# Kernel tuning notes

Measured on AMD Instinct MI355X. Metric: run time of the kernel, lower is better.

Reference implementation:

```python
import jax, jax.numpy as jnp
import numpy as np

N = 100000   # nodes
E = 800000   # edges
IN, H, OUT = 128, 128, 100  # in_channels, hidden_channels, out_channels


def _layernorm(x, g, b, eps=1e-5):
    m = jnp.mean(x, axis=-1, keepdims=True)
    v = jnp.var(x, axis=-1, keepdims=True)
    return (x - m) * jax.lax.rsqrt(v + eps) * g + b


def _sage_mean(x, src, dst, wl, bl, wr, n):
    # PyG SAGEConv(aggr='mean'): lin_l(mean_j x_j) + lin_r(x)
    s = jax.ops.segment_sum(x[src], dst, num_segments=n)               # [n, d]
    cnt = jax.ops.segment_sum(jnp.ones_like(dst, jnp.float32), dst, num_segments=n)
    aggr = s / jnp.maximum(cnt, 1.0)[:, None]
    return aggr @ wl + bl + x @ wr


def _sage_max(x, src, dst, wl, bl, wr, n):
    # PyG SAGEConv(aggr='max'): lin_l(max_j x_j) + lin_r(x); empty segments -> 0
    m = jax.ops.segment_max(x[src], dst, num_segments=n)               # [n, d]
    m = jnp.where(jnp.isfinite(m), m, 0.0)
    return m @ wl + bl + x @ wr


def setup_inputs() -> dict:
    key = jax.random.key(0)
    ks = jax.random.split(key, 16)

    def w(k, shape):
        fan_in = shape[0]
        return jax.random.normal(k, shape, jnp.float32) * (1.0 / np.sqrt(fan_in))

    inp = {
        'x': jax.random.normal(ks[0], (N, IN), jnp.float32),
        'src': jax.random.randint(ks[1], (E,), 0, N, jnp.int32),
        'dst': jax.random.randint(ks[2], (E,), 0, N, jnp.int32),
        's1_wl': w(ks[3], (IN, H)), 's1_bl': jnp.zeros((H,), jnp.float32), 's1_wr': w(ks[4], (IN, H)),
        'ln1_g': jnp.ones((H,), jnp.float32), 'ln1_b': jnp.zeros((H,), jnp.float32),
        's2_wl': w(ks[5], (H, 2 * H)), 's2_bl': jnp.zeros((2 * H,), jnp.float32), 's2_wr': w(ks[6], (H, 2 * H)),
        'ln2_g': jnp.ones((2 * H,), jnp.float32), 'ln2_b': jnp.zeros((2 * H,), jnp.float32),
        's3_wl': w(ks[7], (2 * H, H)), 's3_bl': jnp.zeros((H,), jnp.float32), 's3_wr': w(ks[8], (2 * H, H)),
        'ln3_g': jnp.ones((H,), jnp.float32), 'ln3_b': jnp.zeros((H,), jnp.float32),
        'l1_w': w(ks[9], (H, H // 2)), 'l1_b': jnp.zeros((H // 2,), jnp.float32),
        'ln4_g': jnp.ones((H // 2,), jnp.float32), 'ln4_b': jnp.zeros((H // 2,), jnp.float32),
        'lo_w': w(ks[10], (H // 2, OUT)), 'lo_b': jnp.zeros((OUT,), jnp.float32),
    }
    return inp


def reference(x, src, dst,
              s1_wl, s1_bl, s1_wr, ln1_g, ln1_b,
              s2_wl, s2_bl, s2_wr, ln2_g, ln2_b,
              s3_wl, s3_bl, s3_wr, ln3_g, ln3_b,
              l1_w, l1_b, ln4_g, ln4_b, lo_w, lo_b):
    n = x.shape[0]
    h = _sage_mean(x, src, dst, s1_wl, s1_bl, s1_wr, n)
    h = jax.nn.relu(_layernorm(h, ln1_g, ln1_b))          # dropout disabled (eval)
    h = _sage_max(h, src, dst, s2_wl, s2_bl, s2_wr, n)
    h = jax.nn.relu(_layernorm(h, ln2_g, ln2_b))
    h = _sage_mean(h, src, dst, s3_wl, s3_bl, s3_wr, n)
    h = jax.nn.relu(_layernorm(h, ln3_g, ln3_b))
    h = h @ l1_w + l1_b
    h = jax.nn.relu(_layernorm(h, ln4_g, ln4_b))
    return h @ lo_w + lo_b                                 # [N, OUT]
```

## Files before the change

kernel.cpp:

```cpp
#include <hip/hip_runtime.h>
#include <stdint.h>

#define DEV __device__ __forceinline__

typedef __attribute__((ext_vector_type(8))) short bf16x8;
typedef __attribute__((ext_vector_type(4))) float f32x4;

DEV float bf2f(uint16_t u) { return __uint_as_float(((uint32_t)u) << 16); }
DEV uint16_t f2bfbits(float f) {
    uint32_t x = __float_as_uint(f);
    uint32_t r = x + 0x7fffu + ((x >> 16) & 1u);
    return (uint16_t)(r >> 16);
}
DEV void stv(uint16_t* p, float v) { *p = f2bfbits(v); }
DEV void stv(float* p, float v) { *p = v; }

template<int C> DEV void ldbf(const uint16_t* p, float* f);
template<> DEV void ldbf<2>(const uint16_t* p, float* f) {
    uint32_t v = *reinterpret_cast<const uint32_t*>(p);
    f[0] = __uint_as_float(v << 16); f[1] = __uint_as_float(v & 0xffff0000u);
}
template<> DEV void ldbf<4>(const uint16_t* p, float* f) {
    uint2 v = *reinterpret_cast<const uint2*>(p);
    f[0] = __uint_as_float(v.x << 16); f[1] = __uint_as_float(v.x & 0xffff0000u);
    f[2] = __uint_as_float(v.y << 16); f[3] = __uint_as_float(v.y & 0xffff0000u);
}
template<> DEV void ldbf<8>(const uint16_t* p, float* f) {
    uint4 v = *reinterpret_cast<const uint4*>(p);
    f[0] = __uint_as_float(v.x << 16); f[1] = __uint_as_float(v.x & 0xffff0000u);
    f[2] = __uint_as_float(v.y << 16); f[3] = __uint_as_float(v.y & 0xffff0000u);
    f[4] = __uint_as_float(v.z << 16); f[5] = __uint_as_float(v.z & 0xffff0000u);
    f[6] = __uint_as_float(v.w << 16); f[7] = __uint_as_float(v.w & 0xffff0000u);
}

DEV void gl16(const uint16_t* g, uint8_t* l) {
    __builtin_amdgcn_global_load_lds(
        (const __attribute__((address_space(1))) uint32_t*)g,
        (__attribute__((address_space(3))) uint32_t*)l, 16, 0, 0);
}

template<int N> DEV void vwait() {
    if constexpr (N == 0)      asm volatile("s_waitcnt vmcnt(0)" ::: "memory");
    else if constexpr (N == 3) asm volatile("s_waitcnt vmcnt(3)" ::: "memory");
    else if constexpr (N == 4) asm volatile("s_waitcnt vmcnt(4)" ::: "memory");
    else if constexpr (N == 6) asm volatile("s_waitcnt vmcnt(6)" ::: "memory");
    else                       asm volatile("s_waitcnt vmcnt(0)" ::: "memory");
}

__global__ void k_count(const int* __restrict__ dst, int e, int* __restrict__ deg) {
    int i = blockIdx.x * 256 + threadIdx.x;
    if (i < e) atomicAdd(&deg[dst[i]], 1);
}

__global__ void k_block_sums(const int* __restrict__ deg, int n, int* __restrict__ bsum) {
    __shared__ int sm[256];
    int base = blockIdx.x * 1024;
    int s = 0;
    for (int i = threadIdx.x; i < 1024; i += 256) {
        int g = base + i;
        if (g < n) s += deg[g];
    }
    sm[threadIdx.x] = s; __syncthreads();
    for (int o = 128; o > 0; o >>= 1) {
        if (threadIdx.x < o) sm[threadIdx.x] += sm[threadIdx.x + o];
        __syncthreads();
    }
    if (threadIdx.x == 0) bsum[blockIdx.x] = sm[0];
}

__global__ void k_scan_bsums(int* bsum, int nb) {
    __shared__ int sm[256];
    int t = threadIdx.x;
    int v = (t < nb) ? bsum[t] : 0;
    sm[t] = v; __syncthreads();
    for (int o = 1; o < 256; o <<= 1) {
        int add = (t >= o) ? sm[t - o] : 0;
        __syncthreads();
        sm[t] += add;
        __syncthreads();
    }
    if (t < nb) bsum[t] = (t == 0) ? 0 : sm[t - 1];
}

__global__ void k_scan_final(const int* __restrict__ deg, int n,
                             const int* __restrict__ bsum, int* __restrict__ offs,
                             int* __restrict__ cursor) {
    __shared__ int sm[256];
    int t = threadIdx.x;
    int i0 = blockIdx.x * 1024 + t * 4;
    int d0 = (i0     < n) ? deg[i0]     : 0;
    int d1 = (i0 + 1 < n) ? deg[i0 + 1] : 0;
    int d2 = (i0 + 2 < n) ? deg[i0 + 2] : 0;
    int d3 = (i0 + 3 < n) ? deg[i0 + 3] : 0;
    int ts = d0 + d1 + d2 + d3;
    sm[t] = ts; __syncthreads();
    for (int o = 1; o < 256; o <<= 1) {
        int add = (t >= o) ? sm[t - o] : 0;
        __syncthreads();
        sm[t] += add;
        __syncthreads();
    }
    int e0 = bsum[blockIdx.x] + ((t == 0) ? 0 : sm[t - 1]);
    int e1 = e0 + d0, e2 = e1 + d1, e3 = e2 + d2, e4 = e3 + d3;
    if (i0     < n) { offs[i0]     = e0; cursor[i0]     = e0; }
    if (i0 + 1 < n) { offs[i0 + 1] = e1; cursor[i0 + 1] = e1; }
    if (i0 + 2 < n) { offs[i0 + 2] = e2; cursor[i0 + 2] = e2; }
    if (i0 + 3 < n) { offs[i0 + 3] = e3; cursor[i0 + 3] = e3; }
    if (i0 <= n - 1 && n - 1 < i0 + 4) offs[n] = e4;
}

__global__ void k_scatter(const int* __restrict__ src, const int* __restrict__ dst, int e,
                          int* __restrict__ cursor, int* __restrict__ csr) {
    int i = blockIdx.x * 256 + threadIdx.x;
    if (i < e) {
        int p = atomicAdd(&cursor[dst[i]], 1);
        csr[p] = src[i];
    }
}

__global__ void k_f2b(const float* __restrict__ in, uint16_t* __restrict__ o, int n4) {
    int i = blockIdx.x * 256 + threadIdx.x;
    if (i < n4) {
        float4 v = reinterpret_cast<const float4*>(in)[i];
        uint2 w;
        w.x = f2bfbits(v.x) | ((uint32_t)f2bfbits(v.y) << 16);
        w.y = f2bfbits(v.z) | ((uint32_t)f2bfbits(v.w) << 16);
        reinterpret_cast<uint2*>(o)[i] = w;
    }
}

struct PrepSeg { const float* W; uint16_t* wt; int K, Dreal, ncols, koff, noff, Dtot, start, end; };
struct PrepAll { PrepSeg s[8]; };

__global__ void k_prep_all(PrepAll P, int total) {
    int idx = blockIdx.x * 256 + threadIdx.x;
    if (idx >= total) return;
#pragma unroll
    for (int i = 0; i < 8; ++i) {
        if (idx >= P.s[i].start && idx < P.s[i].end) {
            int loc = idx - P.s[i].start;
            int K = P.s[i].K;
            int nn = loc / K, k = loc - nn * K;
            float v = (nn < P.s[i].Dreal) ? P.s[i].W[(size_t)k * P.s[i].Dreal + nn] : 0.f;
            int c = P.s[i].noff + nn;
            int kk = P.s[i].koff + k;
            P.s[i].wt[((size_t)(kk >> 3) * P.s[i].Dtot + c) * 8 + (kk & 7)] = f2bfbits(v);
        }
    }
}

__global__ __launch_bounds__(256) void k_aggr_max(const uint16_t* __restrict__ X,
                                                  const int* __restrict__ offs,
                                                  const int* __restrict__ csr,
                                                  int n, uint16_t* __restrict__ out) {
    int sl = threadIdx.x & 15;
    int node = blockIdx.x * 16 + (threadIdx.x >> 4);
    if (node >= n) return;
    int beg = offs[node], end = offs[node + 1];
    float acc[8] = {};
    const size_t loff = (size_t)sl * 8;
    int i = beg;
    for (; i + 3 < end; i += 4) {
        int s0 = csr[i], s1 = csr[i + 1], s2 = csr[i + 2], s3 = csr[i + 3];
        float f0[8], f1[8], f2[8], f3[8];
        ldbf<8>(X + (size_t)s0 * 128 + loff, f0);
        ldbf<8>(X + (size_t)s1 * 128 + loff, f1);
        ldbf<8>(X + (size_t)s2 * 128 + loff, f2);
        ldbf<8>(X + (size_t)s3 * 128 + loff, f3);
#pragma unroll
        for (int c = 0; c < 8; c++)
            acc[c] = fmaxf(acc[c], fmaxf(fmaxf(f0[c], f1[c]), fmaxf(f2[c], f3[c])));
    }
    for (; i < end; ++i) {
        int s = csr[i];
        float f[8];
        ldbf<8>(X + (size_t)s * 128 + loff, f);
#pragma unroll
        for (int c = 0; c < 8; c++) acc[c] = fmaxf(acc[c], f[c]);
    }
    uint4 v;
    v.x = f2bfbits(acc[0]) | ((uint32_t)f2bfbits(acc[1]) << 16);
    v.y = f2bfbits(acc[2]) | ((uint32_t)f2bfbits(acc[3]) << 16);
    v.z = f2bfbits(acc[4]) | ((uint32_t)f2bfbits(acc[5]) << 16);
    v.w = f2bfbits(acc[6]) | ((uint32_t)f2bfbits(acc[7]) << 16);
    *reinterpret_cast<uint4*>(out + (size_t)node * 128 + loff) = v;
}

__global__ __launch_bounds__(256) void k_aggr_ln(const uint16_t* __restrict__ YZ,
                                                 const int* __restrict__ offs,
                                                 const int* __restrict__ csr,
                                                 const float* __restrict__ g,
                                                 const float* __restrict__ b,
                                                 int n, uint16_t* __restrict__ out) {
    int sl = threadIdx.x & 15;
    int node = blockIdx.x * 16 + (threadIdx.x >> 4);
    if (node >= n) return;
    int beg = offs[node], end = offs[node + 1];
    float a[8] = {};
    const size_t loff = (size_t)sl * 8;
    int i = beg;
    for (; i + 3 < end; i += 4) {
        int s0 = csr[i], s1 = csr[i + 1], s2 = csr[i + 2], s3 = csr[i + 3];
        float f0[8], f1[8], f2[8], f3[8];
        ldbf<8>(YZ + (size_t)s0 * 256 + loff, f0);
        ldbf<8>(YZ + (size_t)s1 * 256 + loff, f1);
        ldbf<8>(YZ + (size_t)s2 * 256 + loff, f2);
        ldbf<8>(YZ + (size_t)s3 * 256 + loff, f3);
#pragma unroll
        for (int c = 0; c < 8; c++) a[c] += (f0[c] + f1[c]) + (f2[c] + f3[c]);
    }
    for (; i < end; ++i) {
        int s = csr[i];
        float f[8];
        ldbf<8>(YZ + (size_t)s * 256 + loff, f);
#pragma unroll
        for (int c = 0; c < 8; c++) a[c] += f[c];
    }
    int d = end - beg; if (d < 1) d = 1;
    float scale = 1.f / (float)d;
    float z[8];
    ldbf<8>(YZ + (size_t)node * 256 + 128 + loff, z);
    float v[8];
#pragma unroll
    for (int c = 0; c < 8; c++) v[c] = a[c] * scale + z[c];
    float s = 0.f, s2 = 0.f;
#pragma unroll
    for (int c = 0; c < 8; c++) { s += v[c]; s2 += v[c] * v[c]; }
#pragma unroll
    for (int o = 1; o < 16; o <<= 1) { s += __shfl_xor(s, o); s2 += __shfl_xor(s2, o); }
    float mean = s * (1.f / 128.f);
    float var = s2 * (1.f / 128.f) - mean * mean;
    float inv = rsqrtf(var + 1e-5f);
    float y[8];
#pragma unroll
    for (int c = 0; c < 8; c++)
        y[c] = fmaxf((v[c] - mean) * inv * g[loff + c] + b[loff + c], 0.f);
    uint4 w;
    w.x = f2bfbits(y[0]) | ((uint32_t)f2bfbits(y[1]) << 16);
    w.y = f2bfbits(y[2]) | ((uint32_t)f2bfbits(y[3]) << 16);
    w.z = f2bfbits(y[4]) | ((uint32_t)f2bfbits(y[5]) << 16);
    w.w = f2bfbits(y[6]) | ((uint32_t)f2bfbits(y[7]) << 16);
    *reinterpret_cast<uint4*>(out + (size_t)node * 128 + loff) = w;
}

template<int KPER, int DOUT, int DB, bool DUAL, bool LN, bool ZBIAS, typename TO>
__global__ __launch_bounds__(256) void k_mf(const uint16_t* __restrict__ A0,
                                            const uint16_t* __restrict__ A1,
                                            const uint16_t* __restrict__ WT,
                                            const float* __restrict__ bias,
                                            const float* __restrict__ g,
                                            const float* __restrict__ bvec,
                                            int n, TO* __restrict__ out) {
    constexpr int KEFF = KPER * (DUAL ? 2 : 1);
    constexpr int NST = KEFF / 32;
    constexpr int NF = DB / 16;
    constexpr int WPL = DB * 16;
    constexpr int AB = 8192;
    constexpr int WB = DB * 64;
    constexpr int HB = DB / 64;
    constexpr int L  = 2 + HB;
    __shared__ __align__(16) uint8_t lds[3][AB + WB];

    int tid = threadIdx.x;
    int lane = tid & 63, wid = tid >> 6;
    int lr = lane & 15, kb = lane >> 4;
    int row0 = blockIdx.x * 128;
    int wrow = wid * 32;

    auto stage = [&](int kt, uint8_t* buf) {
        const uint16_t* Asel = A0; int kk = kt;
        if (DUAL && kt >= KPER) { Asel = A1; kk = kt - KPER; }
        uint8_t* aB = buf;
        uint8_t* wB = buf + AB;
#pragma unroll
        for (int j = 0; j < 2; ++j) {
            int p = wid * 2 + j, cb = p >> 1, h = p & 1;
            int grow = row0 + h * 64 + lane; if (grow >= n) grow = n - 1;
            gl16(Asel + (size_t)grow * KPER + kk + cb * 8, aB + cb * 2048 + h * 1024);
        }
#pragma unroll
        for (int j = 0; j < HB; ++j) {
            int p = wid * HB + j, cb = p / HB, h = p % HB;
            int plane = (kt >> 3) + cb;
            gl16(WT + ((size_t)plane * DB + h * 64 + lane) * 8, wB + cb * WPL + h * 1024);
        }
    };

    f32x4 acc[2][NF] = {};
    stage(0, lds[0]);
    if constexpr (NST > 1) stage(32, lds[1]);

#pragma unroll
    for (int s = 0; s < NST; ++s) {
        if (s < NST - 1) vwait<L>(); else vwait<0>();
        __builtin_amdgcn_s_barrier();
        __builtin_amdgcn_sched_barrier(0);
        if (s + 2 < NST) stage((s + 2) * 32, lds[(s + 2) % 3]);
        const uint8_t* aB = lds[s % 3];
        const uint8_t* wB = lds[s % 3] + AB;
        bf16x8 af0 = *reinterpret_cast<const bf16x8*>(aB + kb * 2048 + (wrow + lr) * 16);
        bf16x8 af1 = *reinterpret_cast<const bf16x8*>(aB + kb * 2048 + (wrow + 16 + lr) * 16);
#pragma unroll
        for (int nf = 0; nf < NF; ++nf) {
            bf16x8 wf = *reinterpret_cast<const bf16x8*>(wB + kb * WPL + (nf * 16 + lr) * 16);
            acc[0][nf] = __builtin_amdgcn_mfma_f32_16x16x32_bf16(af0, wf, acc[0][nf], 0, 0, 0);
            acc[1][nf] = __builtin_amdgcn_mfma_f32_16x16x32_bf16(af1, wf, acc[1][nf], 0, 0, 0);
        }
    }

#pragma unroll
    for (int nf = 0; nf < NF; ++nf) {
        int col = nf * 16 + lr;
        float bsv;
        if constexpr (ZBIAS) {
            bsv = (col >= DOUT / 2) ? bias[col - DOUT / 2] : 0.f;
        } else {
            bsv = (DB == DOUT || col < DOUT) ? bias[col] : 0.f;
        }
#pragma unroll
        for (int r = 0; r < 4; ++r) { acc[0][nf][r] += bsv; acc[1][nf][r] += bsv; }
    }
    if constexpr (LN) {
        float gv[NF], bv2[NF];
#pragma unroll
        for (int nf = 0; nf < NF; ++nf) {
            int col = nf * 16 + lr;
            gv[nf] = g[col]; bv2[nf] = bvec[col];
        }
#pragma unroll
        for (int m = 0; m < 2; ++m) {
            float s[4], s2[4];
#pragma unroll
            for (int r = 0; r < 4; ++r) { s[r] = 0.f; s2[r] = 0.f; }
#pragma unroll
            for (int nf = 0; nf < NF; ++nf)
#pragma unroll
                for (int r = 0; r < 4; ++r) { float v = acc[m][nf][r]; s[r] += v; s2[r] += v * v; }
#pragma unroll
            for (int r = 0; r < 4; ++r) {
#pragma unroll
                for (int o = 1; o < 16; o <<= 1) {
                    s[r] += __shfl_xor(s[r], o);
                    s2[r] += __shfl_xor(s2[r], o);
                }
                float mean = s[r] / DOUT;
                float var = s2[r] / DOUT - mean * mean;
                float inv = rsqrtf(var + 1e-5f);
#pragma unroll
                for (int nf = 0; nf < NF; ++nf) {
                    float y = (acc[m][nf][r] - mean) * inv * gv[nf] + bv2[nf];
                    acc[m][nf][r] = fmaxf(y, 0.f);
                }
            }
        }
    }
#pragma unroll
    for (int m = 0; m < 2; ++m)
#pragma unroll
        for (int r = 0; r < 4; ++r) {
            int row = row0 + wrow + m * 16 + kb * 4 + r;
            if (row < n) {
#pragma unroll
                for (int nf = 0; nf < NF; ++nf) {
                    int col = nf * 16 + lr;
                    if (DB == DOUT || col < DOUT)
                        stv(out + (size_t)row * DOUT + col, acc[m][nf][r]);
                }
            }
        }
}

__global__ __launch_bounds__(256) void k_tail(const uint16_t* __restrict__ A,
                                              const uint16_t* __restrict__ WT4,
                                              const float* __restrict__ b4,
                                              const float* __restrict__ g4,
                                              const float* __restrict__ bv4,
                                              const uint16_t* __restrict__ WT5,
                                              const float* __restrict__ b5,
                                              int n, float* __restrict__ out) {
    __shared__ __align__(16) uint8_t lds[3][8192 + 4096];
    __shared__ __align__(16) uint8_t w5L[16384];
    __shared__ __align__(16) uint8_t h4L[16384];

    int tid = threadIdx.x;
    int lane = tid & 63, wid = tid >> 6;
    int lr = lane & 15, kb = lane >> 4;
    int row0 = blockIdx.x * 128;
    int wrow = wid * 32;

    auto stage = [&](int kt, uint8_t* buf) {
        uint8_t* aB = buf;
        uint8_t* wB = buf + 8192;
#pragma unroll
        for (int j = 0; j < 2; ++j) {
            int p = wid * 2 + j, cb = p >> 1, h = p & 1;
            int grow = row0 + h * 64 + lane; if (grow >= n) grow = n - 1;
            gl16(A + (size_t)grow * 128 + kt + cb * 8, aB + cb * 2048 + h * 1024);
        }
        gl16(WT4 + ((size_t)((kt >> 3) + wid) * 64 + lane) * 8, wB + wid * 1024);
    };

#pragma unroll
    for (int j = 0; j < 4; ++j) {
        int p = wid * 4 + j, cb = p >> 1, h = p & 1;
        gl16(WT5 + ((size_t)cb * 128 + h * 64 + lane) * 8, w5L + cb * 2048 + h * 1024);
    }

    f32x4 acc1[2][4] = {};
    stage(0, lds[0]);
    stage(32, lds[1]);

#pragma unroll
    for (int s = 0; s < 4; ++s) {
        if (s < 3) vwait<3>(); else vwait<0>();
        __builtin_amdgcn_s_barrier();
        __builtin_amdgcn_sched_barrier(0);
        if (s + 2 < 4) stage((s + 2) * 32, lds[(s + 2) % 3]);
        const uint8_t* aB = lds[s % 3];
        const uint8_t* wB = lds[s % 3] + 8192;
        bf16x8 af0 = *reinterpret_cast<const bf16x8*>(aB + kb * 2048 + (wrow + lr) * 16);
        bf16x8 af1 = *reinterpret_cast<const bf16x8*>(aB + kb * 2048 + (wrow + 16 + lr) * 16);
#pragma unroll
        for (int nf = 0; nf < 4; ++nf) {
            bf16x8 wf = *reinterpret_cast<const bf16x8*>(wB + kb * 1024 + (nf * 16 + lr) * 16);
            acc1[0][nf] = __builtin_amdgcn_mfma_f32_16x16x32_bf16(af0, wf, acc1[0][nf], 0, 0, 0);
            acc1[1][nf] = __builtin_amdgcn_mfma_f32_16x16x32_bf16(af1, wf, acc1[1][nf], 0, 0, 0);
        }
    }

#pragma unroll
    for (int nf = 0; nf < 4; ++nf) {
        float bsv = b4[nf * 16 + lr];
#pragma unroll
        for (int r = 0; r < 4; ++r) { acc1[0][nf][r] += bsv; acc1[1][nf][r] += bsv; }
    }
    {
        float gv[4], bv2[4];
#pragma unroll
        for (int nf = 0; nf < 4; ++nf) { gv[nf] = g4[nf * 16 + lr]; bv2[nf] = bv4[nf * 16 + lr]; }
#pragma unroll
        for (int m = 0; m < 2; ++m) {
            float s[4] = {}, s2[4] = {};
#pragma unroll
            for (int nf = 0; nf < 4; ++nf)
#pragma unroll
                for (int r = 0; r < 4; ++r) { float v = acc1[m][nf][r]; s[r] += v; s2[r] += v * v; }
#pragma unroll
            for (int r = 0; r < 4; ++r) {
#pragma unroll
                for (int o = 1; o < 16; o <<= 1) { s[r] += __shfl_xor(s[r], o); s2[r] += __shfl_xor(s2[r], o); }
                float mean = s[r] * (1.f / 64.f);
                float var = s2[r] * (1.f / 64.f) - mean * mean;
                float inv = rsqrtf(var + 1e-5f);
#pragma unroll
                for (int nf = 0; nf < 4; ++nf)
                    acc1[m][nf][r] = fmaxf((acc1[m][nf][r] - mean) * inv * gv[nf] + bv2[nf], 0.f);
            }
        }
    }

#pragma unroll
    for (int m = 0; m < 2; ++m)
#pragma unroll
        for (int r = 0; r < 4; ++r) {
            int row = wrow + m * 16 + kb * 4 + r;
#pragma unroll
            for (int nf = 0; nf < 4; ++nf) {
                int col = nf * 16 + lr;
                *reinterpret_cast<uint16_t*>(h4L + ((col >> 3) * 2048 + row * 16 + (col & 7) * 2)) =
                    f2bfbits(acc1[m][nf][r]);
            }
        }
    __syncthreads();

    f32x4 acc2[2][8] = {};
#pragma unroll
    for (int s = 0; s < 2; ++s) {
        bf16x8 af0 = *reinterpret_cast<const bf16x8*>(h4L + (s * 4 + kb) * 2048 + (wrow + lr) * 16);
        bf16x8 af1 = *reinterpret_cast<const bf16x8*>(h4L + (s * 4 + kb) * 2048 + (wrow + 16 + lr) * 16);
#pragma unroll
        for (int nf = 0; nf < 8; ++nf) {
            bf16x8 wf = *reinterpret_cast<const bf16x8*>(w5L + (s * 4 + kb) * 2048 + (nf * 16 + lr) * 16);
            acc2[0][nf] = __builtin_amdgcn_mfma_f32_16x16x32_bf16(af0, wf, acc2[0][nf], 0, 0, 0);
            acc2[1][nf] = __builtin_amdgcn_mfma_f32_16x16x32_bf16(af1, wf, acc2[1][nf], 0, 0, 0);
        }
    }
#pragma unroll
    for (int m = 0; m < 2; ++m)
#pragma unroll
        for (int r = 0; r < 4; ++r) {
            int row = row0 + wrow + m * 16 + kb * 4 + r;
            if (row < n) {
#pragma unroll
                for (int nf = 0; nf < 8; ++nf) {
                    int col = nf * 16 + lr;
                    if (col < 100)
                        out[(size_t)row * 100 + col] = acc2[m][nf][r] + b5[col];
                }
            }
        }
}

extern "C" void kernel_launch(void* const* d_in, const int* in_sizes, int n_in,
                              void* d_out, int out_size, void* d_ws, size_t ws_size,
                              hipStream_t stream) {
    const float* x     = (const float*)d_in[0];
    const int*   src   = (const int*)d_in[1];
    const int*   dst   = (const int*)d_in[2];
    const float* s1_wl = (const float*)d_in[3];
    const float* s1_bl = (const float*)d_in[4];
    const float* s1_wr = (const float*)d_in[5];
    const float* ln1_g = (const float*)d_in[6];
    const float* ln1_b = (const float*)d_in[7];
    const float* s2_wl = (const float*)d_in[8];
    const float* s2_bl = (const float*)d_in[9];
    const float* s2_wr = (const float*)d_in[10];
    const float* ln2_g = (const float*)d_in[11];
    const float* ln2_b = (const float*)d_in[12];
    const float* s3_wl = (const float*)d_in[13];
    const float* s3_bl = (const float*)d_in[14];
    const float* s3_wr = (const float*)d_in[15];
    const float* ln3_g = (const float*)d_in[16];
    const float* ln3_b = (const float*)d_in[17];
    const float* l1_w  = (const float*)d_in[18];
    const float* l1_b  = (const float*)d_in[19];
    const float* ln4_g = (const float*)d_in[20];
    const float* ln4_b = (const float*)d_in[21];
    const float* lo_w  = (const float*)d_in[22];
    const float* lo_b  = (const float*)d_in[23];
    float* out = (float*)d_out;

    const int N = in_sizes[0] / 128;
    const int E = in_sizes[1];
    (void)n_in; (void)out_size; (void)ws_size;

    char* w = (char*)d_ws;
    size_t off = 0;
    auto alloc = [&](size_t bytes) -> void* {
        void* p = w + off;
        off = (off + bytes + 255) & ~(size_t)255;
        return p;
    };
    int* deg    = (int*)alloc((size_t)N * 4);
    int* offs   = (int*)alloc((size_t)(N + 1) * 4);
    int* cursor = (int*)alloc((size_t)N * 4);
    int* bsum   = (int*)alloc(1024 * 4);
    int* csr    = (int*)alloc((size_t)E * 4);
    uint16_t* wt1 = (uint16_t*)alloc(256 * 128 * 2);
    uint16_t* wt2 = (uint16_t*)alloc(256 * 256 * 2);
    uint16_t* wt3 = (uint16_t*)alloc(256 * 256 * 2);
    uint16_t* wt4 = (uint16_t*)alloc(64 * 128 * 2);
    uint16_t* wt5 = (uint16_t*)alloc(128 * 64 * 2);
    uint16_t* xb    = (uint16_t*)alloc((size_t)N * 128 * 2);
    uint16_t* YZ    = (uint16_t*)alloc((size_t)N * 256 * 2);
    uint16_t* h1    = (uint16_t*)alloc((size_t)N * 128 * 2);
    uint16_t* aggrB = (uint16_t*)alloc((size_t)N * 128 * 2);
    uint16_t* h2    = (uint16_t*)alloc((size_t)N * 256 * 2);
    uint16_t* h3    = (uint16_t*)alloc((size_t)N * 128 * 2);

    int gE = (E + 255) / 256;
    int nb = (N + 1023) / 1024;
    int gN16 = (N + 15) / 16;
    int g128 = (N + 127) / 128;

    hipMemsetAsync(deg, 0, (size_t)N * 4, stream);
    k_count<<<gE, 256, 0, stream>>>(dst, E, deg);
    k_block_sums<<<nb, 256, 0, stream>>>(deg, N, bsum);
    k_scan_bsums<<<1, 256, 0, stream>>>(bsum, nb);
    k_scan_final<<<nb, 256, 0, stream>>>(deg, N, bsum, offs, cursor);
    k_scatter<<<gE, 256, 0, stream>>>(src, dst, E, cursor, csr);

    PrepAll P;
    int cum = 0;
    auto seg = [&](int i, const float* W, uint16_t* wt, int K, int Dreal, int ncols,
                   int koff, int noff, int Dtot) {
        P.s[i] = {W, wt, K, Dreal, ncols, koff, noff, Dtot, cum, cum + ncols * K};
        cum += ncols * K;
    };
    seg(0, s1_wl, wt1, 128, 128, 128, 0,   0,   256);
    seg(1, s1_wr, wt1, 128, 128, 128, 0,   128, 256);
    seg(2, s2_wl, wt2, 128, 256, 256, 0,   0,   256);
    seg(3, s2_wr, wt2, 128, 256, 256, 128, 0,   256);
    seg(4, s3_wl, wt3, 256, 128, 128, 0,   0,   256);
    seg(5, s3_wr, wt3, 256, 128, 128, 0,   128, 256);
    seg(6, l1_w,  wt4, 128, 64,  64,  0,   0,   64);
    seg(7, lo_w,  wt5, 64,  100, 128, 0,   0,   128);
    k_prep_all<<<(cum + 255) / 256, 256, 0, stream>>>(P, cum);

    k_f2b<<<(N * 128 / 4 + 255) / 256, 256, 0, stream>>>(x, xb, N * 128 / 4);

    k_mf<128, 256, 256, false, false, true, uint16_t><<<g128, 256, 0, stream>>>(
        xb, nullptr, wt1, s1_bl, nullptr, nullptr, N, YZ);
    k_aggr_ln<<<gN16, 256, 0, stream>>>(YZ, offs, csr, ln1_g, ln1_b, N, h1);

    k_aggr_max<<<gN16, 256, 0, stream>>>(h1, offs, csr, N, aggrB);
    k_mf<128, 256, 256, true, true, false, uint16_t><<<g128, 256, 0, stream>>>(
        aggrB, h1, wt2, s2_bl, ln2_g, ln2_b, N, h2);

    k_mf<256, 256, 256, false, false, true, uint16_t><<<g128, 256, 0, stream>>>(
        h2, nullptr, wt3, s3_bl, nullptr, nullptr, N, YZ);
    k_aggr_ln<<<gN16, 256, 0, stream>>>(YZ, offs, csr, ln3_g, ln3_b, N, h3);

    k_tail<<<g128, 256, 0, stream>>>(h3, wt4, l1_b, ln4_g, ln4_b, wt5, lo_b, N, out);
}
```

Measured before the change: 347.3 us.

## Preload whole swizzled A row panel into LDS and halve GEMM block rows

```diff
diff --git a/kernel.cpp b/kernel.cpp
--- a/kernel.cpp
+++ b/kernel.cpp
@@ -16,15 +16,6 @@
 DEV void stv(float* p, float v) { *p = v; }
 
 template<int C> DEV void ldbf(const uint16_t* p, float* f);
-template<> DEV void ldbf<2>(const uint16_t* p, float* f) {
-    uint32_t v = *reinterpret_cast<const uint32_t*>(p);
-    f[0] = __uint_as_float(v << 16); f[1] = __uint_as_float(v & 0xffff0000u);
-}
-template<> DEV void ldbf<4>(const uint16_t* p, float* f) {
-    uint2 v = *reinterpret_cast<const uint2*>(p);
-    f[0] = __uint_as_float(v.x << 16); f[1] = __uint_as_float(v.x & 0xffff0000u);
-    f[2] = __uint_as_float(v.y << 16); f[3] = __uint_as_float(v.y & 0xffff0000u);
-}
 template<> DEV void ldbf<8>(const uint16_t* p, float* f) {
     uint4 v = *reinterpret_cast<const uint4*>(p);
     f[0] = __uint_as_float(v.x << 16); f[1] = __uint_as_float(v.x & 0xffff0000u);
@@ -243,7 +234,7 @@
     *reinterpret_cast<uint4*>(out + (size_t)node * 128 + loff) = w;
 }
 
-template<int KPER, int DOUT, int DB, bool DUAL, bool LN, bool ZBIAS, typename TO>
+template<int KPER, int DOUT, bool DUAL, bool LN, bool ZBIAS, typename TO>
 __global__ __launch_bounds__(256) void k_mf(const uint16_t* __restrict__ A0,
                                             const uint16_t* __restrict__ A1,
                                             const uint16_t* __restrict__ WT,
@@ -251,60 +242,71 @@
                                             const float* __restrict__ g,
                                             const float* __restrict__ bvec,
                                             int n, TO* __restrict__ out) {
+    constexpr int DB = 256;
     constexpr int KEFF = KPER * (DUAL ? 2 : 1);
     constexpr int NST = KEFF / 32;
     constexpr int NF = DB / 16;
     constexpr int WPL = DB * 16;
-    constexpr int AB = 8192;
     constexpr int WB = DB * 64;
     constexpr int HB = DB / 64;
-    constexpr int L  = 2 + HB;
-    __shared__ __align__(16) uint8_t lds[3][AB + WB];
+    constexpr int RB = KPER * 2;
+    constexpr int PAN = 64 * RB;
+    constexpr int PCH = PAN / 1024;
+    constexpr int NPAN = DUAL ? 2 : 1;
+    __shared__ __align__(16) uint8_t aP[NPAN * PAN];
+    __shared__ __align__(16) uint8_t wL[3][WB];
 
     int tid = threadIdx.x;
     int lane = tid & 63, wid = tid >> 6;
     int lr = lane & 15, kb = lane >> 4;
-    int row0 = blockIdx.x * 128;
-    int wrow = wid * 32;
-
-    auto stage = [&](int kt, uint8_t* buf) {
-        const uint16_t* Asel = A0; int kk = kt;
-        if (DUAL && kt >= KPER) { Asel = A1; kk = kt - KPER; }
-        uint8_t* aB = buf;
-        uint8_t* wB = buf + AB;
-#pragma unroll
-        for (int j = 0; j < 2; ++j) {
-            int p = wid * 2 + j, cb = p >> 1, h = p & 1;
-            int grow = row0 + h * 64 + lane; if (grow >= n) grow = n - 1;
-            gl16(Asel + (size_t)grow * KPER + kk + cb * 8, aB + cb * 2048 + h * 1024);
-        }
+    int row0 = blockIdx.x * 64;
+
+    for (int c = wid; c < NPAN * PCH; c += 4) {
+        int pan = c / PCH, cc = c % PCH;
+        const uint16_t* Asrc = (DUAL && pan) ? A1 : A0;
+        int rloc, colb;
+        if constexpr (RB == 256) { rloc = cc * 4 + (lane >> 4); colb = (lane & 15) * 16; }
+        else                     { rloc = cc * 2 + (lane >> 5); colb = (lane & 31) * 16; }
+        int grow = row0 + rloc; if (grow >= n) grow = n - 1;
+        gl16((const uint16_t*)((const uint8_t*)Asrc + (size_t)grow * RB + (colb ^ ((rloc & 7) << 4))),
+             aP + (size_t)c * 1024);
+    }
+
+    auto stageW = [&](int kt, uint8_t* buf) {
 #pragma unroll
         for (int j = 0; j < HB; ++j) {
             int p = wid * HB + j, cb = p / HB, h = p % HB;
             int plane = (kt >> 3) + cb;
-            gl16(WT + ((size_t)plane * DB + h * 64 + lane) * 8, wB + cb * WPL + h * 1024);
+            gl16(WT + ((size_t)plane * DB + h * 64 + lane) * 8, buf + cb * WPL + h * 1024);
         }
     };
 
-    f32x4 acc[2][NF] = {};
-    stage(0, lds[0]);
-    if constexpr (NST > 1) stage(32, lds[1]);
-
+    stageW(0, wL[0]);
+    if constexpr (NST > 1) stageW(32, wL[1]);
+    vwait<0>();
+    __builtin_amdgcn_s_barrier();
+    __builtin_amdgcn_sched_barrier(0);
+
+    f32x4 acc[NF] = {};
 #pragma unroll
     for (int s = 0; s < NST; ++s) {
-        if (s < NST - 1) vwait<L>(); else vwait<0>();
-        __builtin_amdgcn_s_barrier();
-        __builtin_amdgcn_sched_barrier(0);
-        if (s + 2 < NST) stage((s + 2) * 32, lds[(s + 2) % 3]);
-        const uint8_t* aB = lds[s % 3];
-        const uint8_t* wB = lds[s % 3] + AB;
-        bf16x8 af0 = *reinterpret_cast<const bf16x8*>(aB + kb * 2048 + (wrow + lr) * 16);
-        bf16x8 af1 = *reinterpret_cast<const bf16x8*>(aB + kb * 2048 + (wrow + 16 + lr) * 16);
+        if (s > 0) {
+            if (s < NST - 1) vwait<4>(); else vwait<0>();
+            __builtin_amdgcn_s_barrier();
+            __builtin_amdgcn_sched_barrier(0);
+        }
+        if (s + 2 < NST) stageW((s + 2) * 32, wL[(s + 2) % 3]);
+        int kt = s * 32;
+        const uint8_t* pan = aP; int kk = kt;
+        if (DUAL && kt >= KPER) { pan = aP + PAN; kk = kt - KPER; }
+        int ar = wid * 16 + lr;
+        bf16x8 af = *reinterpret_cast<const bf16x8*>(
+            pan + (size_t)ar * RB + (((kk + kb * 8) * 2) ^ ((ar & 7) << 4)));
+        const uint8_t* wB = wL[s % 3];
 #pragma unroll
         for (int nf = 0; nf < NF; ++nf) {
             bf16x8 wf = *reinterpret_cast<const bf16x8*>(wB + kb * WPL + (nf * 16 + lr) * 16);
-            acc[0][nf] = __builtin_amdgcn_mfma_f32_16x16x32_bf16(af0, wf, acc[0][nf], 0, 0, 0);
-            acc[1][nf] = __builtin_amdgcn_mfma_f32_16x16x32_bf16(af1, wf, acc[1][nf], 0, 0, 0);
+            acc[nf] = __builtin_amdgcn_mfma_f32_16x16x32_bf16(af, wf, acc[nf], 0, 0, 0);
         }
     }
 
@@ -315,10 +317,10 @@
         if constexpr (ZBIAS) {
             bsv = (col >= DOUT / 2) ? bias[col - DOUT / 2] : 0.f;
         } else {
-            bsv = (DB == DOUT || col < DOUT) ? bias[col] : 0.f;
-        }
-#pragma unroll
-        for (int r = 0; r < 4; ++r) { acc[0][nf][r] += bsv; acc[1][nf][r] += bsv; }
+            bsv = (col < DOUT) ? bias[col] : 0.f;
+        }
+#pragma unroll
+        for (int r = 0; r < 4; ++r) acc[nf][r] += bsv;
     }
     if constexpr (LN) {
         float gv[NF], bv2[NF];
@@ -327,47 +329,42 @@
             int col = nf * 16 + lr;
             gv[nf] = g[col]; bv2[nf] = bvec[col];
         }
-#pragma unroll
-        for (int m = 0; m < 2; ++m) {
-            float s[4], s2[4];
-#pragma unroll
-            for (int r = 0; r < 4; ++r) { s[r] = 0.f; s2[r] = 0.f; }
-#pragma unroll
-            for (int nf = 0; nf < NF; ++nf)
-#pragma unroll
-                for (int r = 0; r < 4; ++r) { float v = acc[m][nf][r]; s[r] += v; s2[r] += v * v; }
-#pragma unroll
-            for (int r = 0; r < 4; ++r) {
-#pragma unroll
-                for (int o = 1; o < 16; o <<= 1) {
-                    s[r] += __shfl_xor(s[r], o);
-                    s2[r] += __shfl_xor(s2[r], o);
-                }
-                float mean = s[r] / DOUT;
-                float var = s2[r] / DOUT - mean * mean;
-                float inv = rsqrtf(var + 1e-5f);
-#pragma unroll
-                for (int nf = 0; nf < NF; ++nf) {
-                    float y = (acc[m][nf][r] - mean) * inv * gv[nf] + bv2[nf];
-                    acc[m][nf][r] = fmaxf(y, 0.f);
-                }
+        float s[4], s2[4];
+#pragma unroll
+        for (int r = 0; r < 4; ++r) { s[r] = 0.f; s2[r] = 0.f; }
+#pragma unroll
+        for (int nf = 0; nf < NF; ++nf)
+#pragma unroll
+            for (int r = 0; r < 4; ++r) { float v = acc[nf][r]; s[r] += v; s2[r] += v * v; }
+#pragma unroll
+        for (int r = 0; r < 4; ++r) {
+#pragma unroll
+            for (int o = 1; o < 16; o <<= 1) {
+                s[r] += __shfl_xor(s[r], o);
+                s2[r] += __shfl_xor(s2[r], o);
             }
-        }
-    }
-#pragma unroll
-    for (int m = 0; m < 2; ++m)
-#pragma unroll
-        for (int r = 0; r < 4; ++r) {
-            int row = row0 + wrow + m * 16 + kb * 4 + r;
-            if (row < n) {
-#pragma unroll
-                for (int nf = 0; nf < NF; ++nf) {
-                    int col = nf * 16 + lr;
-                    if (DB == DOUT || col < DOUT)
-                        stv(out + (size_t)row * DOUT + col, acc[m][nf][r]);
-                }
+            float mean = s[r] / DOUT;
+            float var = s2[r] / DOUT - mean * mean;
+            float inv = rsqrtf(var + 1e-5f);
+#pragma unroll
+            for (int nf = 0; nf < NF; ++nf) {
+                float y = (acc[nf][r] - mean) * inv * gv[nf] + bv2[nf];
+                acc[nf][r] = fmaxf(y, 0.f);
             }
         }
+    }
+#pragma unroll
+    for (int r = 0; r < 4; ++r) {
+        int row = row0 + wid * 16 + kb * 4 + r;
+        if (row < n) {
+#pragma unroll
+            for (int nf = 0; nf < NF; ++nf) {
+                int col = nf * 16 + lr;
+                if (col < DOUT)
+                    stv(out + (size_t)row * DOUT + col, acc[nf][r]);
+            }
+        }
+    }
 }
 
 __global__ __launch_bounds__(256) void k_tail(const uint16_t* __restrict__ A,
@@ -561,6 +558,7 @@
     int gE = (E + 255) / 256;
     int nb = (N + 1023) / 1024;
     int gN16 = (N + 15) / 16;
+    int g64  = (N + 63) / 64;
     int g128 = (N + 127) / 128;
 
     hipMemsetAsync(deg, 0, (size_t)N * 4, stream);
@@ -589,15 +587,15 @@
 
     k_f2b<<<(N * 128 / 4 + 255) / 256, 256, 0, stream>>>(x, xb, N * 128 / 4);
 
-    k_mf<128, 256, 256, false, false, true, uint16_t><<<g128, 256, 0, stream>>>(
+    k_mf<128, 256, false, false, true, uint16_t><<<g64, 256, 0, stream>>>(
         xb, nullptr, wt1, s1_bl, nullptr, nullptr, N, YZ);
     k_aggr_ln<<<gN16, 256, 0, stream>>>(YZ, offs, csr, ln1_g, ln1_b, N, h1);
 
     k_aggr_max<<<gN16, 256, 0, stream>>>(h1, offs, csr, N, aggrB);
-    k_mf<128, 256, 256, true, true, false, uint16_t><<<g128, 256, 0, stream>>>(
+    k_mf<128, 256, true, true, false, uint16_t><<<g64, 256, 0, stream>>>(
         aggrB, h1, wt2, s2_bl, ln2_g, ln2_b, N, h2);
 
-    k_mf<256, 256, 256, false, false, true, uint16_t><<<g128, 256, 0, stream>>>(
+    k_mf<256, 256, false, false, true, uint16_t><<<g64, 256, 0, stream>>>(
         h2, nullptr, wt3, s3_bl, nullptr, nullptr, N, YZ);
     k_aggr_ln<<<gN16, 256, 0, stream>>>(YZ, offs, csr, ln3_g, ln3_b, N, h3);
 
```

Measured after the change: 359.7 us. 1.04x slower.

## Add panel-staged MFMA GEMM kernel for layer-3 projection with 64-row tiles

Applied to the files above, without the earlier changes.

```diff
diff --git a/kernel.cpp b/kernel.cpp
--- a/kernel.cpp
+++ b/kernel.cpp
@@ -16,15 +16,6 @@
 DEV void stv(float* p, float v) { *p = v; }
 
 template<int C> DEV void ldbf(const uint16_t* p, float* f);
-template<> DEV void ldbf<2>(const uint16_t* p, float* f) {
-    uint32_t v = *reinterpret_cast<const uint32_t*>(p);
-    f[0] = __uint_as_float(v << 16); f[1] = __uint_as_float(v & 0xffff0000u);
-}
-template<> DEV void ldbf<4>(const uint16_t* p, float* f) {
-    uint2 v = *reinterpret_cast<const uint2*>(p);
-    f[0] = __uint_as_float(v.x << 16); f[1] = __uint_as_float(v.x & 0xffff0000u);
-    f[2] = __uint_as_float(v.y << 16); f[3] = __uint_as_float(v.y & 0xffff0000u);
-}
 template<> DEV void ldbf<8>(const uint16_t* p, float* f) {
     uint4 v = *reinterpret_cast<const uint4*>(p);
     f[0] = __uint_as_float(v.x << 16); f[1] = __uint_as_float(v.x & 0xffff0000u);
@@ -368,6 +359,99 @@
                 }
             }
         }
+}
+
+template<int KPER, int DOUT, bool ZBIAS>
+__global__ __launch_bounds__(256) void k_mfp(const uint16_t* __restrict__ A0,
+                                             const uint16_t* __restrict__ WT,
+                                             const float* __restrict__ bias,
+                                             int n, uint16_t* __restrict__ out) {
+    constexpr int DB = 256;
+    constexpr int NST = KPER / 32;
+    constexpr int NF = DB / 16;
+    constexpr int WPL = DB * 16;
+    constexpr int WB = DB * 64;
+    constexpr int HB = DB / 64;
+    constexpr int RB = KPER * 2;
+    constexpr int PAN = 64 * RB;
+    constexpr int PCH = PAN / 1024;
+    __shared__ __align__(16) uint8_t aP[PAN];
+    __shared__ __align__(16) uint8_t wL[3][WB];
+
+    int tid = threadIdx.x;
+    int lane = tid & 63, wid = tid >> 6;
+    int lr = lane & 15, kb = lane >> 4;
+    int row0 = blockIdx.x * 64;
+
+    for (int c = wid; c < PCH; c += 4) {
+        int rloc, colb;
+        if constexpr (RB == 256) { rloc = c * 4 + (lane >> 4); colb = (lane & 15) * 16; }
+        else                     { rloc = c * 2 + (lane >> 5); colb = (lane & 31) * 16; }
+        int grow = row0 + rloc; if (grow >= n) grow = n - 1;
+        gl16((const uint16_t*)((const uint8_t*)A0 + (size_t)grow * RB + (colb ^ ((rloc & 7) << 4))),
+             aP + (size_t)c * 1024);
+    }
+
+    auto stageW = [&](int kt, uint8_t* buf) {
+#pragma unroll
+        for (int j = 0; j < HB; ++j) {
+            int p = wid * HB + j, cb = p / HB, h = p % HB;
+            int plane = (kt >> 3) + cb;
+            gl16(WT + ((size_t)plane * DB + h * 64 + lane) * 8, buf + cb * WPL + h * 1024);
+        }
+    };
+
+    stageW(0, wL[0]);
+    if constexpr (NST > 1) stageW(32, wL[1]);
+    vwait<0>();
+    __builtin_amdgcn_s_barrier();
+    __builtin_amdgcn_sched_barrier(0);
+
+    f32x4 acc[NF] = {};
+#pragma unroll
+    for (int s = 0; s < NST; ++s) {
+        if (s > 0) {
+            if (s < NST - 1) vwait<4>(); else vwait<0>();
+            __builtin_amdgcn_s_barrier();
+            __builtin_amdgcn_sched_barrier(0);
+        }
+        if (s + 2 < NST) stageW((s + 2) * 32, wL[(s + 2) % 3]);
+        int kk = s * 32;
+        int ar = wid * 16 + lr;
+        bf16x8 af = *reinterpret_cast<const bf16x8*>(
+            aP + (size_t)ar * RB + (((kk + kb * 8) * 2) ^ ((ar & 7) << 4)));
+        const uint8_t* wB = wL[s % 3];
+#pragma unroll
+        for (int nf = 0; nf < NF; ++nf) {
+            bf16x8 wf = *reinterpret_cast<const bf16x8*>(wB + kb * WPL + (nf * 16 + lr) * 16);
+            acc[nf] = __builtin_amdgcn_mfma_f32_16x16x32_bf16(af, wf, acc[nf], 0, 0, 0);
+        }
+    }
+
+#pragma unroll
+    for (int nf = 0; nf < NF; ++nf) {
+        int col = nf * 16 + lr;
+        float bsv;
+        if constexpr (ZBIAS) {
+            bsv = (col >= DOUT / 2) ? bias[col - DOUT / 2] : 0.f;
+        } else {
+            bsv = (col < DOUT) ? bias[col] : 0.f;
+        }
+#pragma unroll
+        for (int r = 0; r < 4; ++r) acc[nf][r] += bsv;
+    }
+#pragma unroll
+    for (int r = 0; r < 4; ++r) {
+        int row = row0 + wid * 16 + kb * 4 + r;
+        if (row < n) {
+#pragma unroll
+            for (int nf = 0; nf < NF; ++nf) {
+                int col = nf * 16 + lr;
+                if (col < DOUT)
+                    stv(out + (size_t)row * DOUT + col, acc[nf][r]);
+            }
+        }
+    }
 }
 
 __global__ __launch_bounds__(256) void k_tail(const uint16_t* __restrict__ A,
@@ -561,6 +645,7 @@
     int gE = (E + 255) / 256;
     int nb = (N + 1023) / 1024;
     int gN16 = (N + 15) / 16;
+    int g64  = (N + 63) / 64;
     int g128 = (N + 127) / 128;
 
     hipMemsetAsync(deg, 0, (size_t)N * 4, stream);
@@ -597,8 +682,7 @@
     k_mf<128, 256, 256, true, true, false, uint16_t><<<g128, 256, 0, stream>>>(
         aggrB, h1, wt2, s2_bl, ln2_g, ln2_b, N, h2);
 
-    k_mf<256, 256, 256, false, false, true, uint16_t><<<g128, 256, 0, stream>>>(
-        h2, nullptr, wt3, s3_bl, nullptr, nullptr, N, YZ);
+    k_mfp<256, 256, true><<<g64, 256, 0, stream>>>(h2, wt3, s3_bl, N, YZ);
     k_aggr_ln<<<gN16, 256, 0, stream>>>(YZ, offs, csr, ln3_g, ln3_b, N, h3);
 
     k_tail<<<g128, 256, 0, stream>>>(h3, wt4, l1_b, ln4_g, ln4_b, wt5, lo_b, N, out);
```

Result: slower. 358.1 us (+3.1%).
